# Kernel optimization log

Measured on AMD Instinct MI355X. Metric: run time of the kernel, lower is better.

The kernel has to match this reference:

```python
import jax, jax.numpy as jnp
import numpy as np

N_EMBEDS = 1024
N_HEADS = 16
HEAD_DIM = N_EMBEDS // N_HEADS
SCALE = HEAD_DIM ** (-0.5)
B, T = 2, 2048


def setup_inputs() -> dict:
    key = jax.random.key(0)
    k1, k2, k3, k4 = jax.random.split(key, 4)
    x = jax.random.normal(k1, (B, T, N_EMBEDS), dtype=jnp.float32)
    # Glorot-uniform-style init like keras Dense defaults (scale irrelevant for correctness)
    w_qkv = jax.random.normal(k2, (N_EMBEDS, 3 * N_EMBEDS), dtype=jnp.float32) * (N_EMBEDS ** -0.5)
    w_proj = jax.random.normal(k3, (N_EMBEDS, N_EMBEDS), dtype=jnp.float32) * (N_EMBEDS ** -0.5)
    b_proj = jnp.zeros((N_EMBEDS,), dtype=jnp.float32)
    return {"x": x, "w_qkv": w_qkv, "w_proj": w_proj, "b_proj": b_proj}


def reference(x, w_qkv, w_proj, b_proj):
    Bc, Tc, D = x.shape
    qkv = x @ w_qkv                                   # [B,T,3D]
    q, k, v = jnp.split(qkv, 3, axis=-1)
    def heads(t):
        return t.reshape(Bc, Tc, N_HEADS, HEAD_DIM).transpose(0, 2, 1, 3)  # [B,H,T,hd]
    q, k, v = heads(q), heads(k), heads(v)
    att = jnp.einsum("bhqd,bhkd->bhqk", q, k) * SCALE  # [B,H,T,T]
    causal = jnp.tril(jnp.ones((Tc, Tc), dtype=bool))[None, None]
    att = jnp.where(causal, att, jnp.float32(-1e9))
    att = jax.nn.softmax(att, axis=-1)
    out = jnp.einsum("bhqk,bhkd->bhqd", att, v)        # [B,H,T,hd]
    out = out.transpose(0, 2, 1, 3).reshape(Bc, Tc, D)
    return out @ w_proj + b_proj
```

## Files before the change

### kernel.cpp

```cpp
#include <hip/hip_runtime.h>
#include <hip/hip_bf16.h>


typedef __bf16 bf16;
typedef float f32x4 __attribute__((ext_vector_type(4)));
typedef float f32x16 __attribute__((ext_vector_type(16)));
typedef bf16 bf16x4 __attribute__((ext_vector_type(4)));
typedef bf16 bf16x8 __attribute__((ext_vector_type(8)));

#define B_ 2
#define T_ 2048
#define D_ 1024
#define H_ 16
#define HD_ 64

__device__ __forceinline__ f32x16 mfma32(bf16x8 a, bf16x8 b, f32x16 c) {
    return __builtin_amdgcn_mfma_f32_32x32x16_bf16(a, b, c, 0, 0, 0);
}

__device__ __forceinline__ void gload16(void* l, const void* g) {
    __builtin_amdgcn_global_load_lds(
        (const __attribute__((address_space(1))) unsigned int*)g,
        (__attribute__((address_space(3))) unsigned int*)l, 16, 0, 0);
}

__device__ __forceinline__ f32x16 z16() {
    f32x16 v;
#pragma unroll
    for (int i = 0; i < 16; ++i) v[i] = 0.f;
    return v;
}

__global__ __launch_bounds__(256) void cast_f32_bf16(const float* __restrict__ in,
                                                     bf16* __restrict__ out, int n4) {
    int i = blockIdx.x * 256 + threadIdx.x;
    if (i < n4) {
        float4 v = ((const float4*)in)[i];
        bf16x4 o = { (bf16)v.x, (bf16)v.y, (bf16)v.z, (bf16)v.w };
        ((bf16x4*)out)[i] = o;
    }
}

__global__ __launch_bounds__(256) void cast_transpose(const float* __restrict__ in,
                                                      bf16* __restrict__ out, int R, int C) {
    __shared__ float tile[32][33];
    int cx = blockIdx.x * 32 + threadIdx.x;
    int r0 = blockIdx.y * 32;
#pragma unroll
    for (int j = 0; j < 32; j += 8)
        tile[threadIdx.y + j][threadIdx.x] = in[(size_t)(r0 + threadIdx.y + j) * C + cx];
    __syncthreads();
    int rx = r0 + threadIdx.x;
    int c0 = blockIdx.x * 32;
#pragma unroll
    for (int j = 0; j < 32; j += 8)
        out[(size_t)(c0 + threadIdx.y + j) * R + rx] = (bf16)tile[threadIdx.x][threadIdx.y + j];
}

__global__ __launch_bounds__(256) void transpose_v(const bf16* __restrict__ vb,
                                                   bf16* __restrict__ vt) {
    __shared__ bf16 st[64 * 65];
    const int bh = blockIdx.y;
    const int t0 = blockIdx.x * 64;
    const int tid = threadIdx.x;
#pragma unroll
    for (int c = 0; c < 2; ++c) {
        int cid = tid + c * 256;
        int r = cid >> 3, col = (cid & 7) * 8;
        bf16x8 v = *(const bf16x8*)&vb[((size_t)bh * T_ + t0 + r) * HD_ + col];
#pragma unroll
        for (int j = 0; j < 8; ++j) st[r * 65 + col + j] = v[j];
    }
    __syncthreads();
#pragma unroll
    for (int c = 0; c < 2; ++c) {
        int cid = tid + c * 256;
        int tg = cid & 7, d = cid >> 3;
        bf16x8 o;
#pragma unroll
        for (int j = 0; j < 8; ++j) o[j] = st[(tg * 8 + j) * 65 + d];
        *(bf16x8*)&vt[((size_t)bh * HD_ + d) * T_ + t0 + tg * 8] = o;
    }
}

template <int MW, int NWN, int EPI>
__global__ __launch_bounds__(256) void gemm_k(
    const bf16* __restrict__ A, const bf16* __restrict__ Bt,
    int M, int N, int K,
    bf16* __restrict__ qb, bf16* __restrict__ kb, bf16* __restrict__ vb,
    const float* __restrict__ bias, float* __restrict__ outf) {
    constexpr int BM = 64 * MW;
    constexpr int BN = 64 * NWN;
    __shared__ bf16 sA[BM * 64];
    __shared__ bf16 sB[BN * 64];
    const int tid = threadIdx.x;
    const int wave = tid >> 6, lane = tid & 63;
    const int ln = lane & 31, hi = lane >> 5;
    const int wr = (wave >> 1) * (32 * MW);
    const int wc = (wave & 1) * (32 * NWN);
    const int m0 = blockIdx.x * BM, n0 = blockIdx.y * BN;

    f32x16 acc[MW][NWN];
#pragma unroll
    for (int mi = 0; mi < MW; ++mi)
#pragma unroll
        for (int ni = 0; ni < NWN; ++ni) acc[mi][ni] = z16();

    for (int k0 = 0; k0 < K; k0 += 64) {
        __syncthreads();
#pragma unroll
        for (int j = 0; j < 2 * MW; ++j) {
            int c = tid + 256 * j;
            int r = c >> 3, g = (c & 7) ^ (r & 7);
            gload16(&sA[c * 8], A + (size_t)(m0 + r) * K + k0 + 8 * g);
        }
#pragma unroll
        for (int j = 0; j < 2 * NWN; ++j) {
            int c = tid + 256 * j;
            int r = c >> 3, g = (c & 7) ^ (r & 7);
            gload16(&sB[c * 8], Bt + (size_t)(n0 + r) * K + k0 + 8 * g);
        }
        __syncthreads();
#pragma unroll
        for (int s = 0; s < 4; ++s) {
            bf16x8 av[MW], bv[NWN];
#pragma unroll
            for (int mi = 0; mi < MW; ++mi) {
                int r = wr + mi * 32 + ln;
                av[mi] = *(const bf16x8*)((const char*)sA + r * 128 +
                                          ((((s << 1) | hi) ^ (r & 7)) << 4));
            }
#pragma unroll
            for (int ni = 0; ni < NWN; ++ni) {
                int r = wc + ni * 32 + ln;
                bv[ni] = *(const bf16x8*)((const char*)sB + r * 128 +
                                          ((((s << 1) | hi) ^ (r & 7)) << 4));
            }
#pragma unroll
            for (int mi = 0; mi < MW; ++mi)
#pragma unroll
                for (int ni = 0; ni < NWN; ++ni)
                    acc[mi][ni] = mfma32(av[mi], bv[ni], acc[mi][ni]);
        }
    }

#pragma unroll
    for (int mi = 0; mi < MW; ++mi)
#pragma unroll
        for (int ni = 0; ni < NWN; ++ni)
#pragma unroll
            for (int r = 0; r < 16; ++r) {
                int row = m0 + wr + mi * 32 + (r & 3) + 8 * (r >> 2) + 4 * hi;
                int col = n0 + wc + ni * 32 + ln;
                float v = acc[mi][ni][r];
                if (EPI == 0) {
                    int part = col >> 10, h = (col >> 6) & 15, d = col & 63;
                    int b = row >> 11, t = row & (T_ - 1);
                    size_t idx = ((size_t)(b * H_ + h) * T_ + t) * HD_ + d;
                    bf16* dst = (part == 0) ? qb : (part == 1) ? kb : vb;
                    dst[idx] = (bf16)v;
                } else {
                    outf[(size_t)row * N + col] = v + bias[col];
                }
            }
}

__device__ __forceinline__ bf16x8 kread(const char* base, int row, int s, int hi) {
    int b = (row * 128 + s * 32 + hi * 16) ^ ((row & 7) << 4);
    return *(const bf16x8*)(base + b);
}
__device__ __forceinline__ bf16x8 vread(const char* base, int row, int s, int hi) {
    int sw = (row & 7) << 4;
    int b0 = (row * 128 + s * 32 + hi * 8) ^ sw;
    int b1 = (row * 128 + s * 32 + hi * 8 + 16) ^ sw;
    bf16x4 lo = *(const bf16x4*)(base + b0);
    bf16x4 hi4 = *(const bf16x4*)(base + b1);
    return __builtin_shufflevector(lo, hi4, 0, 1, 2, 3, 4, 5, 6, 7);
}

__global__ __launch_bounds__(256) void attn_kernel(
    const bf16* __restrict__ qb, const bf16* __restrict__ kb,
    const bf16* __restrict__ vtb, bf16* __restrict__ ob) {
    __shared__ bf16 sK2[2][4096];
    __shared__ bf16 sV2[2][4096];

    const int bx = blockIdx.x;
    const int bh = bx & 31;
    const int qt = (bx < 256) ? ((bx >> 5) & 7) : (15 - ((bx >> 5) & 7));
    const int b = bh >> 4, h = bh & 15;
    const int tid = threadIdx.x, wave = tid >> 6, lane = tid & 63;
    const int ln = lane & 31, hi = lane >> 5;
    const int qs = qt * 128 + wave * 32;
    const int qrow = qs + ln;
    const int ntiles = 2 * qt + 2;

    const bf16* Qg = qb + (size_t)bh * (T_ * HD_);
    const bf16* Kg = kb + (size_t)bh * (T_ * HD_);
    const bf16* Vtg = vtb + (size_t)bh * (HD_ * T_);

    bf16x8 qf[4];
#pragma unroll
    for (int s = 0; s < 4; ++s) {
        bf16x8 v = *(const bf16x8*)&Qg[(size_t)qrow * HD_ + s * 16 + hi * 8];
#pragma unroll
        for (int e = 0; e < 8; ++e) v[e] = (bf16)((float)v[e] * 0.1803368801f);
        qf[s] = v;
    }

    const int srow = tid >> 3;
    const int scol = (tid & 7) * 8;
    const int kw0 = (srow * 128 + (tid & 7) * 16) ^ ((srow & 7) << 4);
    const int kw1 = ((srow + 32) * 128 + (tid & 7) * 16) ^ ((srow & 7) << 4);

    {
        bf16x8 k0 = *(const bf16x8*)&Kg[(size_t)srow * HD_ + scol];
        bf16x8 k1 = *(const bf16x8*)&Kg[(size_t)(srow + 32) * HD_ + scol];
        bf16x8 v0 = *(const bf16x8*)&Vtg[(size_t)srow * T_ + scol];
        bf16x8 v1 = *(const bf16x8*)&Vtg[(size_t)(srow + 32) * T_ + scol];
        *(bf16x8*)((char*)sK2[0] + kw0) = k0;
        *(bf16x8*)((char*)sK2[0] + kw1) = k1;
        *(bf16x8*)((char*)sV2[0] + kw0) = v0;
        *(bf16x8*)((char*)sV2[0] + kw1) = v1;
    }
    __syncthreads();

    const float NINF = -__builtin_inff();
    f32x16 oA = z16(), oB = z16();
    float mR = NINF, lR = 0.f;
    int cur = 0;

    for (int t = 0; t < ntiles; ++t) {
        bf16x8 kr0, kr1, vr0, vr1;
        const bool pf = (t + 1) < ntiles;
        if (pf) {
            int kv0 = (t + 1) * 64;
            kr0 = *(const bf16x8*)&Kg[(size_t)(kv0 + srow) * HD_ + scol];
            kr1 = *(const bf16x8*)&Kg[(size_t)(kv0 + srow + 32) * HD_ + scol];
            vr0 = *(const bf16x8*)&Vtg[(size_t)srow * T_ + kv0 + scol];
            vr1 = *(const bf16x8*)&Vtg[(size_t)(srow + 32) * T_ + kv0 + scol];
        }

        if (64 * t <= qs + 31) {
            const char* kbase = (const char*)sK2[cur];
            const char* vbase = (const char*)sV2[cur];

            f32x16 p0 = z16(), p1 = z16();
#pragma unroll
            for (int s = 0; s < 4; ++s) {
                bf16x8 a0 = kread(kbase, ln, s, hi);
                bf16x8 a1 = kread(kbase, ln + 32, s, hi);
                p0 = mfma32(a0, qf[s], p0);
                p1 = mfma32(a1, qf[s], p1);
            }

            if (64 * t + 63 > qs) {
                int kvb = 64 * t + 4 * hi;
#pragma unroll
                for (int r = 0; r < 16; ++r) {
                    int kvr = kvb + (r & 3) + 8 * (r >> 2);
                    if (kvr > qrow) p0[r] = NINF;
                    if (kvr + 32 > qrow) p1[r] = NINF;
                }
            }

            float mx0 = NINF, mx1 = NINF, mx2 = NINF, mx3 = NINF;
#pragma unroll
            for (int r = 0; r < 16; r += 4) {
                mx0 = fmaxf(mx0, p0[r]);     mx1 = fmaxf(mx1, p0[r + 1]);
                mx2 = fmaxf(mx2, p0[r + 2]); mx3 = fmaxf(mx3, p0[r + 3]);
                mx0 = fmaxf(mx0, p1[r]);     mx1 = fmaxf(mx1, p1[r + 1]);
                mx2 = fmaxf(mx2, p1[r + 2]); mx3 = fmaxf(mx3, p1[r + 3]);
            }
            float pm = fmaxf(fmaxf(mx0, mx1), fmaxf(mx2, mx3));
            pm = fmaxf(pm, __shfl_xor(pm, 32));
            float mnew = fmaxf(mR, pm);
            float fac = exp2f(mR - mnew);
            mR = mnew;
            float s0 = 0.f, s1 = 0.f, s2 = 0.f, s3 = 0.f;
#pragma unroll
            for (int r = 0; r < 16; r += 4) {
                p0[r] = exp2f(p0[r] - mnew);         s0 += p0[r];
                p0[r + 1] = exp2f(p0[r + 1] - mnew); s1 += p0[r + 1];
                p0[r + 2] = exp2f(p0[r + 2] - mnew); s2 += p0[r + 2];
                p0[r + 3] = exp2f(p0[r + 3] - mnew); s3 += p0[r + 3];
                p1[r] = exp2f(p1[r] - mnew);         s0 += p1[r];
                p1[r + 1] = exp2f(p1[r + 1] - mnew); s1 += p1[r + 1];
                p1[r + 2] = exp2f(p1[r + 2] - mnew); s2 += p1[r + 2];
                p1[r + 3] = exp2f(p1[r + 3] - mnew); s3 += p1[r + 3];
            }
            float rs = (s0 + s1) + (s2 + s3);
            rs += __shfl_xor(rs, 32);
            lR = lR * fac + rs;
#pragma unroll
            for (int r = 0; r < 16; ++r) { oA[r] *= fac; oB[r] *= fac; }

            bf16x8 pa0, pa1, pa2, pa3;
#pragma unroll
            for (int e = 0; e < 8; ++e) {
                pa0[e] = (bf16)p0[e];
                pa1[e] = (bf16)p0[8 + e];
                pa2[e] = (bf16)p1[e];
                pa3[e] = (bf16)p1[8 + e];
            }

#pragma unroll
            for (int s = 0; s < 4; ++s) {
                bf16x8 pas = (s == 0) ? pa0 : (s == 1) ? pa1 : (s == 2) ? pa2 : pa3;
                oA = mfma32(vread(vbase, ln, s, hi), pas, oA);
                oB = mfma32(vread(vbase, ln + 32, s, hi), pas, oB);
            }
        }

        if (pf) {
            int nb = cur ^ 1;
            *(bf16x8*)((char*)sK2[nb] + kw0) = kr0;
            *(bf16x8*)((char*)sK2[nb] + kw1) = kr1;
            *(bf16x8*)((char*)sV2[nb] + kw0) = vr0;
            *(bf16x8*)((char*)sV2[nb] + kw1) = vr1;
        }
        __syncthreads();
        cur ^= 1;
    }

    float inv = 1.f / lR;
    bf16* orow = ob + ((size_t)(b * T_ + qrow)) * D_ + h * HD_;
#pragma unroll
    for (int g = 0; g < 4; ++g) {
        bf16x4 w, w2;
#pragma unroll
        for (int j = 0; j < 4; ++j) {
            w[j] = (bf16)(oA[4 * g + j] * inv);
            w2[j] = (bf16)(oB[4 * g + j] * inv);
        }
        *(bf16x4*)&orow[4 * hi + 8 * g] = w;
        *(bf16x4*)&orow[32 + 4 * hi + 8 * g] = w2;
    }
}

extern "C" void kernel_launch(void* const* d_in, const int* in_sizes, int n_in,
                              void* d_out, int out_size, void* d_ws, size_t ws_size,
                              hipStream_t stream) {
    const float* x = (const float*)d_in[0];
    const float* w_qkv = (const float*)d_in[1];
    const float* w_proj = (const float*)d_in[2];
    const float* b_proj = (const float*)d_in[3];
    float* out = (float*)d_out;
    char* ws = (char*)d_ws;

    bf16* xb = (bf16*)(ws);
    bf16* ob = (bf16*)(ws);
    bf16* wqkvt = (bf16*)(ws + 8388608);
    bf16* vtbuf = (bf16*)(ws + 8388608);
    bf16* qbuf = (bf16*)(ws + 16777216);
    bf16* wprojt = (bf16*)(ws + 16777216);
    bf16* kbuf = (bf16*)(ws + 25165824);
    bf16* vbuf = (bf16*)(ws + 33554432);

    cast_f32_bf16<<<4096, 256, 0, stream>>>(x, xb, (B_ * T_ * D_) / 4);
    dim3 tb(32, 8);
    cast_transpose<<<dim3(3 * D_ / 32, D_ / 32), tb, 0, stream>>>(w_qkv, wqkvt, D_, 3 * D_);

    gemm_k<2, 2, 0><<<dim3((B_ * T_) / 128, (3 * D_) / 128), 256, 0, stream>>>(
        xb, wqkvt, B_ * T_, 3 * D_, D_, qbuf, kbuf, vbuf, nullptr, nullptr);

    transpose_v<<<dim3(T_ / 64, B_ * H_), 256, 0, stream>>>(vbuf, vtbuf);

    attn_kernel<<<512, 256, 0, stream>>>(qbuf, kbuf, vtbuf, ob);

    cast_transpose<<<dim3(D_ / 32, D_ / 32), tb, 0, stream>>>(w_proj, wprojt, D_, D_);

    gemm_k<1, 2, 1><<<dim3((B_ * T_) / 64, D_ / 128), 256, 0, stream>>>(
        ob, wprojt, B_ * T_, D_, D_, nullptr, nullptr, nullptr, b_proj, out);
}
```

Before: 129.9 us.

## Split long causal query tiles across KV segments and add lazy softmax rescale

Query tiles at index 9 and above are split into two KV-range segments, each run as a separate block. Each block writes unnormalized bf16 partial outputs plus running max and sum, and a new merge kernel combines them. This is meant to fix the load imbalance of causal attention on a 512-block grid by launching 736 more evenly sized blocks. The online-softmax rescale is also made lazy: O and l are rescaled only when the row max grows by more than 8 in log2 units. The split costs extra partial-output traffic and an extra kernel launch. Storing partial outputs in bf16 loses some precision, and the lazy rescale lets exponentials reach up to 2^8 before rescaling.

```diff
diff --git a/kernel.cpp b/kernel.cpp
--- a/kernel.cpp
+++ b/kernel.cpp
@@ -13,6 +13,7 @@
 #define D_ 1024
 #define H_ 16
 #define HD_ 64
+#define QSPLIT 9
 
 __device__ __forceinline__ f32x16 mfma32(bf16x8 a, bf16x8 b, f32x16 c) {
     return __builtin_amdgcn_mfma_f32_32x32x16_bf16(a, b, c, 0, 0, 0);
@@ -180,19 +181,29 @@
 
 __global__ __launch_bounds__(256) void attn_kernel(
     const bf16* __restrict__ qb, const bf16* __restrict__ kb,
-    const bf16* __restrict__ vtb, bf16* __restrict__ ob) {
+    const bf16* __restrict__ vtb, bf16* __restrict__ ob,
+    bf16* __restrict__ oP, float2* __restrict__ mlP) {
     __shared__ bf16 sK2[2][4096];
     __shared__ bf16 sV2[2][4096];
 
-    const int bx = blockIdx.x;
-    const int bh = bx & 31;
-    const int qt = (bx < 256) ? ((bx >> 5) & 7) : (15 - ((bx >> 5) & 7));
+    const int bid = blockIdx.x;
+    const int bh = bid & 31;
+    const int sid = bid >> 5;
+    int qt, seg, t0, t1;
+    if (sid < QSPLIT) {
+        qt = sid; seg = -1; t0 = 0; t1 = 2 * qt + 2;
+    } else {
+        int idx = sid - QSPLIT;
+        qt = QSPLIT + (idx >> 1);
+        seg = idx & 1;
+        if (seg == 0) { t0 = 0; t1 = qt + 1; }
+        else          { t0 = qt + 1; t1 = 2 * qt + 2; }
+    }
     const int b = bh >> 4, h = bh & 15;
     const int tid = threadIdx.x, wave = tid >> 6, lane = tid & 63;
     const int ln = lane & 31, hi = lane >> 5;
     const int qs = qt * 128 + wave * 32;
     const int qrow = qs + ln;
-    const int ntiles = 2 * qt + 2;
 
     const bf16* Qg = qb + (size_t)bh * (T_ * HD_);
     const bf16* Kg = kb + (size_t)bh * (T_ * HD_);
@@ -213,10 +224,11 @@
     const int kw1 = ((srow + 32) * 128 + (tid & 7) * 16) ^ ((srow & 7) << 4);
 
     {
-        bf16x8 k0 = *(const bf16x8*)&Kg[(size_t)srow * HD_ + scol];
-        bf16x8 k1 = *(const bf16x8*)&Kg[(size_t)(srow + 32) * HD_ + scol];
-        bf16x8 v0 = *(const bf16x8*)&Vtg[(size_t)srow * T_ + scol];
-        bf16x8 v1 = *(const bf16x8*)&Vtg[(size_t)(srow + 32) * T_ + scol];
+        int kv0 = t0 * 64;
+        bf16x8 k0 = *(const bf16x8*)&Kg[(size_t)(kv0 + srow) * HD_ + scol];
+        bf16x8 k1 = *(const bf16x8*)&Kg[(size_t)(kv0 + srow + 32) * HD_ + scol];
+        bf16x8 v0 = *(const bf16x8*)&Vtg[(size_t)srow * T_ + kv0 + scol];
+        bf16x8 v1 = *(const bf16x8*)&Vtg[(size_t)(srow + 32) * T_ + kv0 + scol];
         *(bf16x8*)((char*)sK2[0] + kw0) = k0;
         *(bf16x8*)((char*)sK2[0] + kw1) = k1;
         *(bf16x8*)((char*)sV2[0] + kw0) = v0;
@@ -229,9 +241,9 @@
     float mR = NINF, lR = 0.f;
     int cur = 0;
 
-    for (int t = 0; t < ntiles; ++t) {
+    for (int t = t0; t < t1; ++t) {
         bf16x8 kr0, kr1, vr0, vr1;
-        const bool pf = (t + 1) < ntiles;
+        const bool pf = (t + 1) < t1;
         if (pf) {
             int kv0 = (t + 1) * 64;
             kr0 = *(const bf16x8*)&Kg[(size_t)(kv0 + srow) * HD_ + scol];
@@ -273,26 +285,31 @@
             }
             float pm = fmaxf(fmaxf(mx0, mx1), fmaxf(mx2, mx3));
             pm = fmaxf(pm, __shfl_xor(pm, 32));
-            float mnew = fmaxf(mR, pm);
-            float fac = exp2f(mR - mnew);
-            mR = mnew;
+
+            if (__any(pm > mR + 8.f)) {
+                float mnew = fmaxf(mR, pm);
+                float fac = exp2f(mR - mnew);
+                lR *= fac;
+#pragma unroll
+                for (int r = 0; r < 16; ++r) { oA[r] *= fac; oB[r] *= fac; }
+                mR = mnew;
+            }
+
             float s0 = 0.f, s1 = 0.f, s2 = 0.f, s3 = 0.f;
 #pragma unroll
             for (int r = 0; r < 16; r += 4) {
-                p0[r] = exp2f(p0[r] - mnew);         s0 += p0[r];
-                p0[r + 1] = exp2f(p0[r + 1] - mnew); s1 += p0[r + 1];
-                p0[r + 2] = exp2f(p0[r + 2] - mnew); s2 += p0[r + 2];
-                p0[r + 3] = exp2f(p0[r + 3] - mnew); s3 += p0[r + 3];
-                p1[r] = exp2f(p1[r] - mnew);         s0 += p1[r];
-                p1[r + 1] = exp2f(p1[r + 1] - mnew); s1 += p1[r + 1];
-                p1[r + 2] = exp2f(p1[r + 2] - mnew); s2 += p1[r + 2];
-                p1[r + 3] = exp2f(p1[r + 3] - mnew); s3 += p1[r + 3];
+                p0[r] = exp2f(p0[r] - mR);         s0 += p0[r];
+                p0[r + 1] = exp2f(p0[r + 1] - mR); s1 += p0[r + 1];
+                p0[r + 2] = exp2f(p0[r + 2] - mR); s2 += p0[r + 2];
+                p0[r + 3] = exp2f(p0[r + 3] - mR); s3 += p0[r + 3];
+                p1[r] = exp2f(p1[r] - mR);         s0 += p1[r];
+                p1[r + 1] = exp2f(p1[r + 1] - mR); s1 += p1[r + 1];
+                p1[r + 2] = exp2f(p1[r + 2] - mR); s2 += p1[r + 2];
+                p1[r + 3] = exp2f(p1[r + 3] - mR); s3 += p1[r + 3];
             }
             float rs = (s0 + s1) + (s2 + s3);
             rs += __shfl_xor(rs, 32);
-            lR = lR * fac + rs;
-#pragma unroll
-            for (int r = 0; r < 16; ++r) { oA[r] *= fac; oB[r] *= fac; }
+            lR += rs;
 
             bf16x8 pa0, pa1, pa2, pa3;
 #pragma unroll
@@ -322,18 +339,68 @@
         cur ^= 1;
     }
 
-    float inv = 1.f / lR;
-    bf16* orow = ob + ((size_t)(b * T_ + qrow)) * D_ + h * HD_;
-#pragma unroll
-    for (int g = 0; g < 4; ++g) {
-        bf16x4 w, w2;
-#pragma unroll
-        for (int j = 0; j < 4; ++j) {
-            w[j] = (bf16)(oA[4 * g + j] * inv);
-            w2[j] = (bf16)(oB[4 * g + j] * inv);
-        }
-        *(bf16x4*)&orow[4 * hi + 8 * g] = w;
-        *(bf16x4*)&orow[32 + 4 * hi + 8 * g] = w2;
+    if (seg < 0) {
+        float inv = 1.f / lR;
+        bf16* orow = ob + ((size_t)(b * T_ + qrow)) * D_ + h * HD_;
+#pragma unroll
+        for (int g = 0; g < 4; ++g) {
+            bf16x4 w, w2;
+#pragma unroll
+            for (int j = 0; j < 4; ++j) {
+                w[j] = (bf16)(oA[4 * g + j] * inv);
+                w2[j] = (bf16)(oB[4 * g + j] * inv);
+            }
+            *(bf16x4*)&orow[4 * hi + 8 * g] = w;
+            *(bf16x4*)&orow[32 + 4 * hi + 8 * g] = w2;
+        }
+    } else {
+        int row = wave * 32 + ln;
+        size_t sbase = (((size_t)bh * (16 - QSPLIT) + (qt - QSPLIT)) * 2 + seg);
+        bf16* prow = oP + (sbase * 128 + row) * 64;
+#pragma unroll
+        for (int g = 0; g < 4; ++g) {
+            bf16x4 w, w2;
+#pragma unroll
+            for (int j = 0; j < 4; ++j) {
+                w[j] = (bf16)oA[4 * g + j];
+                w2[j] = (bf16)oB[4 * g + j];
+            }
+            *(bf16x4*)&prow[4 * hi + 8 * g] = w;
+            *(bf16x4*)&prow[32 + 4 * hi + 8 * g] = w2;
+        }
+        if (hi == 0) mlP[sbase * 128 + row] = make_float2(mR, lR);
+    }
+}
+
+__global__ __launch_bounds__(256) void attn_merge(
+    const bf16* __restrict__ oP, const float2* __restrict__ mlP,
+    bf16* __restrict__ ob) {
+    constexpr int NQS = 16 - QSPLIT;
+    int gid = blockIdx.x * 256 + threadIdx.x;
+    int bh = gid / (NQS * 128);
+    int rem = gid - bh * (NQS * 128);
+    int qi = rem >> 7, row = rem & 127;
+    int b = bh >> 4, h = bh & 15;
+    int t = (QSPLIT + qi) * 128 + row;
+    size_t sbase = ((size_t)bh * NQS + qi) * 2;
+    float2 ml0 = mlP[(sbase + 0) * 128 + row];
+    float2 ml1 = mlP[(sbase + 1) * 128 + row];
+    float ms = fmaxf(ml0.x, ml1.x);
+    float w0 = exp2f(ml0.x - ms), w1 = exp2f(ml1.x - ms);
+    float inv = 1.f / (ml0.y * w0 + ml1.y * w1);
+    w0 *= inv; w1 *= inv;
+    const bf16* r0 = oP + ((sbase + 0) * 128 + row) * 64;
+    const bf16* r1 = oP + ((sbase + 1) * 128 + row) * 64;
+    bf16* dst = ob + ((size_t)(b * T_ + t)) * D_ + h * HD_;
+#pragma unroll
+    for (int g = 0; g < 8; ++g) {
+        bf16x8 a = *(const bf16x8*)&r0[g * 8];
+        bf16x8 c = *(const bf16x8*)&r1[g * 8];
+        bf16x8 o;
+#pragma unroll
+        for (int j = 0; j < 8; ++j)
+            o[j] = (bf16)((float)a[j] * w0 + (float)c[j] * w1);
+        *(bf16x8*)&dst[g * 8] = o;
     }
 }
 
@@ -355,6 +422,8 @@
     bf16* wprojt = (bf16*)(ws + 16777216);
     bf16* kbuf = (bf16*)(ws + 25165824);
     bf16* vbuf = (bf16*)(ws + 33554432);
+    bf16* oP = (bf16*)(ws + 33554432);
+    float2* mlP = (float2*)(ws + 33554432 + 7340032);
 
     cast_f32_bf16<<<4096, 256, 0, stream>>>(x, xb, (B_ * T_ * D_) / 4);
     dim3 tb(32, 8);
@@ -365,7 +434,8 @@
 
     transpose_v<<<dim3(T_ / 64, B_ * H_), 256, 0, stream>>>(vbuf, vtbuf);
 
-    attn_kernel<<<512, 256, 0, stream>>>(qbuf, kbuf, vtbuf, ob);
+    attn_kernel<<<23 * 32, 256, 0, stream>>>(qbuf, kbuf, vtbuf, ob, oP, mlP);
+    attn_merge<<<112, 256, 0, stream>>>(oP, mlP, ob);
 
     cast_transpose<<<dim3(D_ / 32, D_ / 32), tb, 0, stream>>>(w_proj, wprojt, D_, D_);
 
```

After: 135.7 us. +4.5%, slower.
